# Kernel optimization log

Hardware: AMD Instinct MI355X
Metric: run time of the kernel (lower is better)

## Reference

```python
import jax, jax.numpy as jnp
import numpy as np

N_NODES = 100000
N_EDGES = 1600000
F_IN = 256
HID = 32
HEADS = 4
N_CLASS = 40
NEG_SLOPE = 0.2  # DGL GATConv default leaky_relu slope


def _gat_layer(x, src, dst, W, attn_l, attn_r, bias, num_nodes):
    """One DGL-style GATConv layer.
    x: [N, F_in]; W: [F_in, H*D]; attn_l/attn_r: [H, D]; bias: [H, D].
    Returns [N, H, D].
    """
    H, D = attn_l.shape
    h = (x @ W).reshape(-1, H, D)                      # [N, H, D]
    el = jnp.einsum('nhd,hd->nh', h, attn_l)           # [N, H]
    er = jnp.einsum('nhd,hd->nh', h, attn_r)           # [N, H]
    e = el[src] + er[dst]                              # [E, H]
    e = jnp.where(e > 0, e, NEG_SLOPE * e)             # leaky_relu
    # segment softmax over edges grouped by destination node
    m = jax.ops.segment_max(e, dst, num_segments=num_nodes)   # [N, H]
    ex = jnp.exp(e - m[dst])                           # [E, H]
    denom = jax.ops.segment_sum(ex, dst, num_segments=num_nodes)  # [N, H]
    alpha = ex / (denom[dst] + 1e-9)                   # [E, H]
    msg = h[src] * alpha[:, :, None]                   # [E, H, D]
    out = jax.ops.segment_sum(msg, dst, num_segments=num_nodes)   # [N, H, D]
    return out + bias[None, :, :]


def setup_inputs() -> dict:
    key = jax.random.key(0)
    ks = jax.random.split(key, 16)
    x = jax.random.normal(ks[0], (N_NODES, F_IN), dtype=jnp.float32)
    edge_src = jax.random.randint(ks[1], (N_EDGES,), 0, N_NODES, dtype=jnp.int32)
    edge_dst = jax.random.randint(ks[2], (N_EDGES,), 0, N_NODES, dtype=jnp.int32)

    def glorot(k, shape):
        fan_in, fan_out = shape[0], int(np.prod(shape[1:]))
        lim = float(np.sqrt(6.0 / (fan_in + fan_out)))
        return jax.random.uniform(k, shape, jnp.float32, -lim, lim)

    d1 = HID * HEADS  # 128
    inp = {
        'x': x, 'edge_src': edge_src, 'edge_dst': edge_dst,
        'W1': glorot(ks[3], (F_IN, HEADS * HID)),
        'al1': glorot(ks[4], (HEADS, HID)),
        'ar1': glorot(ks[5], (HEADS, HID)),
        'b1': jnp.zeros((HEADS, HID), jnp.float32),
        'W2': glorot(ks[6], (d1, HEADS * HID)),
        'al2': glorot(ks[7], (HEADS, HID)),
        'ar2': glorot(ks[8], (HEADS, HID)),
        'b2': jnp.zeros((HEADS, HID), jnp.float32),
        'W3': glorot(ks[9], (d1, 1 * N_CLASS)),
        'al3': glorot(ks[10], (1, N_CLASS)),
        'ar3': glorot(ks[11], (1, N_CLASS)),
        'b3': jnp.zeros((1, N_CLASS), jnp.float32),
    }
    return inp


def reference(x, edge_src, edge_dst, W1, al1, ar1, b1, W2, al2, ar2, b2, W3, al3, ar3, b3):
    N = x.shape[0]
    h = _gat_layer(x, edge_src, edge_dst, W1, al1, ar1, b1, N).reshape(N, -1)
    h = jax.nn.elu(h)  # act='elu'
    h = _gat_layer(h, edge_src, edge_dst, W2, al2, ar2, b2, N).reshape(N, -1)
    h = jax.nn.elu(h)
    out = _gat_layer(h, edge_src, edge_dst, W3, al3, ar3, b3, N).reshape(N, -1)
    return out
```

## Files before the change

### kernel.cpp

```cpp
#include <hip/hip_runtime.h>
#include <math.h>


#define HEADS 4
#define HID   32
#define NCLS  40
#define BSH   8
#define CH    4096
#define BCAP  6144

typedef __attribute__((ext_vector_type(8))) short bf16x8;
typedef __attribute__((ext_vector_type(4))) float f32x4;

static __device__ __forceinline__ unsigned short f2bf(float f) {
    unsigned int u = __float_as_uint(f);
    u += 0x7fffu + ((u >> 16) & 1u);
    return (unsigned short)(u >> 16);
}
static __device__ __forceinline__ float bflo(unsigned int v) {
    return __uint_as_float(v << 16);
}
static __device__ __forceinline__ float bfhi(unsigned int v) {
    return __uint_as_float(v & 0xffff0000u);
}
static __device__ __forceinline__ unsigned int pack2bf(float lo, float hi) {
    return (unsigned int)f2bf(lo) | ((unsigned int)f2bf(hi) << 16);
}


__global__ __launch_bounds__(256) void prep_all(const float* __restrict__ W1,
                                                const float* __restrict__ W2,
                                                const float* __restrict__ W3,
                                                unsigned short* __restrict__ Wt1,
                                                unsigned short* __restrict__ Wt2,
                                                unsigned short* __restrict__ Wt3,
                                                int NBUCK, int* __restrict__ bcur) {
    int g = blockIdx.x * 256 + threadIdx.x;
    if (g < 32768) {
        int m = g >> 8, k = g & 255;
        Wt1[g] = f2bf(W1[(size_t)k * 128 + m]);
    } else if (g < 49152) {
        int g2 = g - 32768;
        int m = g2 >> 7, k = g2 & 127;
        Wt2[g2] = f2bf(W2[(size_t)k * 128 + m]);
    } else if (g < 54272) {
        int g3 = g - 49152;
        int m = g3 >> 7, k = g3 & 127;
        Wt3[g3] = f2bf(W3[(size_t)k * 40 + m]);
    } else if (g - 54272 < NBUCK) {
        int b = g - 54272;
        bcur[b] = b * BCAP;
    }
}


__global__ __launch_bounds__(256) void bucket_partition(const int* __restrict__ src,
                                                        const int* __restrict__ dst, int E,
                                                        int NBUCK, int* __restrict__ bcur,
                                                        unsigned long long* __restrict__ ebuf) {
    __shared__ int h[512];
    __shared__ int base[512];
    int tid = threadIdx.x;
    int e0 = blockIdx.x * CH;
    for (int i = tid; i < NBUCK; i += 256) h[i] = 0;
    __syncthreads();
    #pragma unroll
    for (int l = 0; l < CH / 256; ++l) {
        int g = e0 + l * 256 + tid;
        if (g < E) atomicAdd(&h[dst[g] >> BSH], 1);
    }
    __syncthreads();
    for (int i = tid; i < NBUCK; i += 256) {
        int c = h[i];
        if (c) base[i] = atomicAdd(&bcur[i], c);
    }
    __syncthreads();
    #pragma unroll
    for (int l = 0; l < CH / 256; ++l) {
        int g = e0 + l * 256 + tid;
        if (g < E) {
            int d = dst[g];
            int p = atomicAdd(&base[d >> BSH], 1);
            ebuf[p] = ((unsigned long long)(unsigned)d << 32) | (unsigned)src[g];
        }
    }
}

__global__ __launch_bounds__(256) void bucket_csr(const unsigned long long* __restrict__ ebuf,
                                                  const int* __restrict__ bcur, int N,
                                                  int2* __restrict__ rowbe,
                                                  int* __restrict__ csrc) {
    __shared__ int cnt[256];
    __shared__ int s[256];
    int b = blockIdx.x, tid = threadIdx.x;
    int beg = b * BCAP, end = bcur[b];
    int d0 = b << BSH;
    cnt[tid] = 0;
    __syncthreads();
    for (int i = beg + tid; i < end; i += 256)
        atomicAdd(&cnt[(int)(ebuf[i] >> 32) - d0], 1);
    __syncthreads();
    int v = cnt[tid];
    s[tid] = v;
    __syncthreads();
    for (int off = 1; off < 256; off <<= 1) {
        int t = (tid >= off) ? s[tid - off] : 0;
        __syncthreads();
        s[tid] += t;
        __syncthreads();
    }
    int excl = s[tid] - v;
    int d = d0 + tid;
    if (d < N) rowbe[d] = make_int2(beg + excl, beg + excl + v);
    cnt[tid] = beg + excl;
    __syncthreads();
    for (int i = beg + tid; i < end; i += 256) {
        unsigned long long e = ebuf[i];
        int p = atomicAdd(&cnt[(int)(e >> 32) - d0], 1);
        csrc[p] = (int)(e & 0xffffffffu);
    }
}


template <bool AFP32, bool OBF, bool WIDEN>
__global__ __launch_bounds__(256) void gemm_mfma(const void* __restrict__ Asrc,
                                                 const unsigned short* __restrict__ Wt,
                                                 void* __restrict__ Y,
                                                 int N, int K, int M) {
    constexpr int WRF = WIDEN ? 4 : 2;
    constexpr int WCF = WIDEN ? 4 : 3;
    __shared__ __align__(16) unsigned short As[128][40];
    __shared__ __align__(16) unsigned short Bs[128][40];
    const int t = threadIdx.x;
    const int lane = t & 63, w = t >> 6;
    const int r0 = blockIdx.x * 128;
    const int wrow = WIDEN ? (w >> 1) * 64 : w * 32;
    const int wcol = WIDEN ? (w & 1) * 64 : 0;
    const int srow = t >> 1, shalf = t & 1;
    const int lr = lane & 15, lq = lane >> 4;
    f32x4 acc[WRF][WCF];
    #pragma unroll
    for (int f = 0; f < WRF; ++f)
        #pragma unroll
        for (int g = 0; g < WCF; ++g)
            acc[f][g] = (f32x4){0.f, 0.f, 0.f, 0.f};

    for (int k0 = 0; k0 < K; k0 += 32) {
        {
            int gr = r0 + srow;
            if (gr < N) {
                if constexpr (AFP32) {
                    const float* gp = (const float*)Asrc + (size_t)gr * K + k0 + shalf * 16;
                    float4 f0 = *(const float4*)(gp + 0);
                    float4 f1 = *(const float4*)(gp + 4);
                    float4 f2 = *(const float4*)(gp + 8);
                    float4 f3 = *(const float4*)(gp + 12);
                    *(uint4*)&As[srow][shalf * 16 + 0] =
                        make_uint4(pack2bf(f0.x, f0.y), pack2bf(f0.z, f0.w),
                                   pack2bf(f1.x, f1.y), pack2bf(f1.z, f1.w));
                    *(uint4*)&As[srow][shalf * 16 + 8] =
                        make_uint4(pack2bf(f2.x, f2.y), pack2bf(f2.z, f2.w),
                                   pack2bf(f3.x, f3.y), pack2bf(f3.z, f3.w));
                } else {
                    const uint4* gp = (const uint4*)((const unsigned short*)Asrc +
                                                     (size_t)gr * K + k0 + shalf * 16);
                    *(uint4*)&As[srow][shalf * 16 + 0] = gp[0];
                    *(uint4*)&As[srow][shalf * 16 + 8] = gp[1];
                }
            }
        }
        {
            int col = srow;
            if (col < M) {
                const uint4* gp = (const uint4*)(Wt + (size_t)col * K + k0 + shalf * 16);
                *(uint4*)&Bs[col][shalf * 16 + 0] = gp[0];
                *(uint4*)&Bs[col][shalf * 16 + 8] = gp[1];
            }
        }
        __syncthreads();
        bf16x8 af[WRF], bfr[WCF];
        #pragma unroll
        for (int f = 0; f < WRF; ++f)
            af[f] = *(const bf16x8*)&As[wrow + f * 16 + lr][lq * 8];
        #pragma unroll
        for (int g = 0; g < WCF; ++g)
            bfr[g] = *(const bf16x8*)&Bs[wcol + g * 16 + lr][lq * 8];
        #pragma unroll
        for (int f = 0; f < WRF; ++f)
            #pragma unroll
            for (int g = 0; g < WCF; ++g)
                acc[f][g] = __builtin_amdgcn_mfma_f32_16x16x32_bf16(af[f], bfr[g],
                                                                   acc[f][g], 0, 0, 0);
        __syncthreads();
    }
    #pragma unroll
    for (int f = 0; f < WRF; ++f) {
        #pragma unroll
        for (int g = 0; g < WCF; ++g) {
            int col = wcol + g * 16 + lr;
            if (!WIDEN && col >= M) continue;
            #pragma unroll
            for (int r = 0; r < 4; ++r) {
                int row = r0 + wrow + f * 16 + lq * 4 + r;
                if (row < N) {
                    if constexpr (OBF)
                        ((unsigned short*)Y)[(size_t)row * M + col] = f2bf(acc[f][g][r]);
                    else
                        ((float*)Y)[(size_t)row * M + col] = acc[f][g][r];
                }
            }
        }
    }
}


template <int H, int D, bool BF>
__global__ __launch_bounds__(256) void elr_kernel(const void* __restrict__ hv,
                                                  const float* __restrict__ al,
                                                  const float* __restrict__ ar,
                                                  float* __restrict__ el,
                                                  float* __restrict__ er, int N) {
    int g = blockIdx.x * blockDim.x + threadIdx.x;
    int n = g / H, hh = g % H;
    if (n >= N) return;
    float sl = 0.f, sr = 0.f;
    if constexpr (BF) {
        const unsigned short* hp = (const unsigned short*)hv + (size_t)n * H * D + hh * D;
        #pragma unroll
        for (int d = 0; d < D; d += 8) {
            uint4 u = *(const uint4*)(hp + d);
            float4 a0 = *(const float4*)(al + hh * D + d);
            float4 a1 = *(const float4*)(al + hh * D + d + 4);
            float4 r0 = *(const float4*)(ar + hh * D + d);
            float4 r1 = *(const float4*)(ar + hh * D + d + 4);
            float h0 = bflo(u.x), h1 = bfhi(u.x);
            float h2 = bflo(u.y), h3 = bfhi(u.y);
            float h4 = bflo(u.z), h5 = bfhi(u.z);
            float h6 = bflo(u.w), h7 = bfhi(u.w);
            sl += h0 * a0.x + h1 * a0.y + h2 * a0.z + h3 * a0.w
                + h4 * a1.x + h5 * a1.y + h6 * a1.z + h7 * a1.w;
            sr += h0 * r0.x + h1 * r0.y + h2 * r0.z + h3 * r0.w
                + h4 * r1.x + h5 * r1.y + h6 * r1.z + h7 * r1.w;
        }
    } else {
        const float* hp = (const float*)hv + (size_t)n * H * D + hh * D;
        #pragma unroll
        for (int d = 0; d < D; d += 4) {
            float4 hvv = *(const float4*)(hp + d);
            float4 av = *(const float4*)(al + hh * D + d);
            float4 rv = *(const float4*)(ar + hh * D + d);
            sl += hvv.x * av.x + hvv.y * av.y + hvv.z * av.z + hvv.w * av.w;
            sr += hvv.x * rv.x + hvv.y * rv.y + hvv.z * rv.z + hvv.w * rv.w;
        }
    }
    el[(size_t)n * H + hh] = sl;
    er[(size_t)n * H + hh] = sr;
}


template <int H, int D, bool ELU, bool BFW, bool OB>
__global__ __launch_bounds__(256) void agg_kernel(const void* __restrict__ hsrcv,
                                                  const float* __restrict__ el,
                                                  const float* __restrict__ er,
                                                  const float* __restrict__ bias,
                                                  const int2* __restrict__ rowbe,
                                                  const int* __restrict__ csrc,
                                                  void* __restrict__ outv, int N) {
    constexpr int HD = H * D;
    int wid = (int)(((size_t)blockIdx.x * blockDim.x + threadIdx.x) >> 6);
    int lane = threadIdx.x & 63;
    if (wid >= N) return;
    int eb = BFW ? lane * 2 : lane;
    bool active = BFW || (lane < HD);
    int head = active ? (eb / D) : 0;
    float er_d = er[(size_t)wid * H + head];
    int2 be = rowbe[wid];
    int beg = be.x, end = be.y;
    const unsigned int* hb = (const unsigned int*)hsrcv;
    const float* hf = (const float*)hsrcv;

    float denom = 0.f, a0 = 0.f, a1 = 0.f;

#define AGG_UPDATE(EV, HX, HY)                                                 \
    {                                                                          \
        float e_ = (EV) + er_d;                                                \
        e_ = (e_ > 0.f) ? e_ : 0.2f * e_;                                      \
        float ex_ = __expf(e_);                                                \
        denom += ex_;                                                          \
        a0 = fmaf(ex_, (HX), a0);                                              \
        a1 = fmaf(ex_, (HY), a1);                                              \
    }

    for (int chunk = beg; chunk < end; chunk += 64) {
        int cnt = min(64, end - chunk);
        int cs = (lane < cnt) ? csrc[chunk + lane] : 0;
        int j = 0;
        for (; j + 4 <= cnt; j += 4) {
            int s0 = __shfl(cs, j + 0), s1 = __shfl(cs, j + 1);
            int s2 = __shfl(cs, j + 2), s3 = __shfl(cs, j + 3);
            float e0 = el[(size_t)s0 * H + head];
            float e1 = el[(size_t)s1 * H + head];
            float e2 = el[(size_t)s2 * H + head];
            float e3 = el[(size_t)s3 * H + head];
            float h0x, h0y = 0.f, h1x, h1y = 0.f, h2x, h2y = 0.f, h3x, h3y = 0.f;
            if (BFW) {
                unsigned int v0 = hb[(size_t)s0 * (HD / 2) + lane];
                unsigned int v1 = hb[(size_t)s1 * (HD / 2) + lane];
                unsigned int v2 = hb[(size_t)s2 * (HD / 2) + lane];
                unsigned int v3 = hb[(size_t)s3 * (HD / 2) + lane];
                h0x = bflo(v0); h0y = bfhi(v0);
                h1x = bflo(v1); h1y = bfhi(v1);
                h2x = bflo(v2); h2y = bfhi(v2);
                h3x = bflo(v3); h3y = bfhi(v3);
            } else {
                h0x = active ? hf[(size_t)s0 * HD + eb] : 0.f;
                h1x = active ? hf[(size_t)s1 * HD + eb] : 0.f;
                h2x = active ? hf[(size_t)s2 * HD + eb] : 0.f;
                h3x = active ? hf[(size_t)s3 * HD + eb] : 0.f;
            }
            AGG_UPDATE(e0, h0x, h0y);
            AGG_UPDATE(e1, h1x, h1y);
            AGG_UPDATE(e2, h2x, h2y);
            AGG_UPDATE(e3, h3x, h3y);
        }
        for (; j < cnt; ++j) {
            int s0 = __shfl(cs, j);
            float e0 = el[(size_t)s0 * H + head];
            float hx, hy = 0.f;
            if (BFW) {
                unsigned int v0 = hb[(size_t)s0 * (HD / 2) + lane];
                hx = bflo(v0); hy = bfhi(v0);
            } else {
                hx = active ? hf[(size_t)s0 * HD + eb] : 0.f;
            }
            AGG_UPDATE(e0, hx, hy);
        }
    }
#undef AGG_UPDATE

    float inv = 1.f / (denom + 1e-9f);
    if (BFW) {
        float o0 = a0 * inv + bias[eb];
        float o1 = a1 * inv + bias[eb + 1];
        if (ELU) {
            o0 = (o0 > 0.f) ? o0 : expm1f(o0);
            o1 = (o1 > 0.f) ? o1 : expm1f(o1);
        }
        if constexpr (OB) {
            ((unsigned int*)outv)[(size_t)wid * (HD / 2) + lane] = pack2bf(o0, o1);
        } else {
            *(float2*)((float*)outv + (size_t)wid * HD + eb) = make_float2(o0, o1);
        }
    } else if (active) {
        float o = a0 * inv + bias[eb];
        if (ELU) o = (o > 0.f) ? o : expm1f(o);
        ((float*)outv)[(size_t)wid * HD + eb] = o;
    }
}


extern "C" void kernel_launch(void* const* d_in, const int* in_sizes, int n_in,
                              void* d_out, int out_size, void* d_ws, size_t ws_size,
                              hipStream_t stream) {
    const float* x    = (const float*)d_in[0];
    const int* esrc   = (const int*)d_in[1];
    const int* edst   = (const int*)d_in[2];
    const float* W1   = (const float*)d_in[3];
    const float* al1  = (const float*)d_in[4];
    const float* ar1  = (const float*)d_in[5];
    const float* b1   = (const float*)d_in[6];
    const float* W2   = (const float*)d_in[7];
    const float* al2  = (const float*)d_in[8];
    const float* ar2  = (const float*)d_in[9];
    const float* b2   = (const float*)d_in[10];
    const float* W3   = (const float*)d_in[11];
    const float* al3  = (const float*)d_in[12];
    const float* ar3  = (const float*)d_in[13];
    const float* b3   = (const float*)d_in[14];

    const int FIN = 256;
    const int N = in_sizes[0] / FIN;
    const int E = in_sizes[1];
    const int D1 = HEADS * HID;
    const int NBUCK = (N + 255) >> BSH;

    unsigned short* Abf = (unsigned short*)d_ws;
    unsigned short* Cbf = Abf + (size_t)N * D1;
    float* A32 = (float*)(Cbf + (size_t)N * D1);
    float* el  = A32 + (size_t)N * NCLS;
    float* er  = el + (size_t)N * HEADS;
    int2* rowbe = (int2*)(er + (size_t)N * HEADS);
    int* csrc   = (int*)(rowbe + N);
    int* bcur   = csrc + (size_t)NBUCK * BCAP;
    unsigned short* Wt1 = (unsigned short*)(bcur + NBUCK);
    unsigned short* Wt2 = Wt1 + 128 * 256;
    unsigned short* Wt3 = Wt2 + 128 * 128;
    unsigned long long* ebuf = (unsigned long long*)Abf;

    int WGRID = (int)(((size_t)N * 64 + 255) / 256);
    int PB = (E + CH - 1) / CH;
    int GB = (N + 127) / 128;

    prep_all<<<(54272 + NBUCK + 255) / 256, 256, 0, stream>>>(W1, W2, W3, Wt1, Wt2, Wt3,
                                                              NBUCK, bcur);

    bucket_partition<<<PB, 256, 0, stream>>>(esrc, edst, E, NBUCK, bcur, ebuf);
    bucket_csr<<<NBUCK, 256, 0, stream>>>(ebuf, bcur, N, rowbe, csrc);

    gemm_mfma<true, true, true><<<GB, 256, 0, stream>>>(x, Wt1, Abf, N, FIN, D1);
    elr_kernel<HEADS, HID, true><<<(N * HEADS + 255) / 256, 256, 0, stream>>>(Abf, al1, ar1, el, er, N);
    agg_kernel<HEADS, HID, true, true, true><<<WGRID, 256, 0, stream>>>(Abf, el, er, b1, rowbe, csrc, Cbf, N);

    gemm_mfma<false, true, true><<<GB, 256, 0, stream>>>(Cbf, Wt2, Abf, N, D1, D1);
    elr_kernel<HEADS, HID, true><<<(N * HEADS + 255) / 256, 256, 0, stream>>>(Abf, al2, ar2, el, er, N);
    agg_kernel<HEADS, HID, true, true, true><<<WGRID, 256, 0, stream>>>(Abf, el, er, b2, rowbe, csrc, Cbf, N);

    gemm_mfma<false, false, false><<<GB, 256, 0, stream>>>(Cbf, Wt3, A32, N, D1, NCLS);
    elr_kernel<1, NCLS, false><<<(N + 255) / 256, 256, 0, stream>>>(A32, al3, ar3, el, er, N);
    agg_kernel<1, NCLS, false, false, false><<<WGRID, 256, 0, stream>>>(A32, el, er, b3, rowbe, csrc, d_out, N);
}
```

Baseline: 363.1 us.

## Fold attention projections into GEMM weights and double-buffer GEMM LDS tiles

```diff
diff --git a/kernel.cpp b/kernel.cpp
--- a/kernel.cpp
+++ b/kernel.cpp
@@ -31,24 +31,56 @@
 __global__ __launch_bounds__(256) void prep_all(const float* __restrict__ W1,
                                                 const float* __restrict__ W2,
                                                 const float* __restrict__ W3,
+                                                const float* __restrict__ al1,
+                                                const float* __restrict__ ar1,
+                                                const float* __restrict__ al2,
+                                                const float* __restrict__ ar2,
+                                                const float* __restrict__ al3,
+                                                const float* __restrict__ ar3,
                                                 unsigned short* __restrict__ Wt1,
                                                 unsigned short* __restrict__ Wt2,
                                                 unsigned short* __restrict__ Wt3,
+                                                unsigned short* __restrict__ aw1,
+                                                unsigned short* __restrict__ aw2,
+                                                unsigned short* __restrict__ aw3,
                                                 int NBUCK, int* __restrict__ bcur) {
     int g = blockIdx.x * 256 + threadIdx.x;
     if (g < 32768) {
         int m = g >> 8, k = g & 255;
         Wt1[g] = f2bf(W1[(size_t)k * 128 + m]);
     } else if (g < 49152) {
-        int g2 = g - 32768;
-        int m = g2 >> 7, k = g2 & 127;
-        Wt2[g2] = f2bf(W2[(size_t)k * 128 + m]);
+        int i = g - 32768;
+        int m = i >> 7, k = i & 127;
+        Wt2[i] = f2bf(W2[(size_t)k * 128 + m]);
     } else if (g < 54272) {
-        int g3 = g - 49152;
-        int m = g3 >> 7, k = g3 & 127;
-        Wt3[g3] = f2bf(W3[(size_t)k * 40 + m]);
-    } else if (g - 54272 < NBUCK) {
-        int b = g - 54272;
+        int i = g - 49152;
+        int m = i >> 7, k = i & 127;
+        Wt3[i] = f2bf(W3[(size_t)k * 40 + m]);
+    } else if (g < 56320) {
+        int i = g - 54272;
+        int v = i >> 8, k = i & 255;
+        const float* a = (v < 4) ? al1 : ar1;
+        int h = v & 3;
+        float s = 0.f;
+        for (int d = 0; d < 32; ++d) s += W1[(size_t)k * 128 + h * 32 + d] * a[h * 32 + d];
+        aw1[v * 256 + k] = f2bf(s);
+    } else if (g < 57344) {
+        int i = g - 56320;
+        int v = i >> 7, k = i & 127;
+        const float* a = (v < 4) ? al2 : ar2;
+        int h = v & 3;
+        float s = 0.f;
+        for (int d = 0; d < 32; ++d) s += W2[(size_t)k * 128 + h * 32 + d] * a[h * 32 + d];
+        aw2[v * 128 + k] = f2bf(s);
+    } else if (g < 57600) {
+        int i = g - 57344;
+        int v = i >> 7, k = i & 127;
+        const float* a = v ? ar3 : al3;
+        float s = 0.f;
+        for (int m = 0; m < 40; ++m) s += W3[(size_t)k * 40 + m] * a[m];
+        aw3[v * 128 + k] = f2bf(s);
+    } else if (g - 57600 < NBUCK) {
+        int b = g - 57600;
         bcur[b] = b * BCAP;
     }
 }
@@ -125,12 +157,17 @@
 template <bool AFP32, bool OBF, bool WIDEN>
 __global__ __launch_bounds__(256) void gemm_mfma(const void* __restrict__ Asrc,
                                                  const unsigned short* __restrict__ Wt,
+                                                 const unsigned short* __restrict__ aw,
                                                  void* __restrict__ Y,
+                                                 float* __restrict__ el,
+                                                 float* __restrict__ er,
                                                  int N, int K, int M) {
     constexpr int WRF = WIDEN ? 4 : 2;
     constexpr int WCF = WIDEN ? 4 : 3;
-    __shared__ __align__(16) unsigned short As[128][40];
-    __shared__ __align__(16) unsigned short Bs[128][40];
+    constexpr int BR  = WIDEN ? 144 : 48;
+    constexpr int EBASE = WIDEN ? 128 : 0;
+    __shared__ __align__(16) unsigned short As[2][128][40];
+    __shared__ __align__(16) unsigned short Bs[2][BR][40];
     const int t = threadIdx.x;
     const int lane = t & 63, w = t >> 6;
     const int r0 = blockIdx.x * 128;
@@ -138,123 +175,144 @@
     const int wcol = WIDEN ? (w & 1) * 64 : 0;
     const int srow = t >> 1, shalf = t & 1;
     const int lr = lane & 15, lq = lane >> 4;
+    const bool xw = WIDEN && (w & 1);
+    const int gr = r0 + srow;
+    const bool arow_ok = gr < N;
+    const bool brow_ok = srow < (WIDEN ? M : M + 2);
+
     f32x4 acc[WRF][WCF];
     #pragma unroll
     for (int f = 0; f < WRF; ++f)
         #pragma unroll
         for (int g = 0; g < WCF; ++g)
             acc[f][g] = (f32x4){0.f, 0.f, 0.f, 0.f};
-
-    for (int k0 = 0; k0 < K; k0 += 32) {
-        {
-            int gr = r0 + srow;
-            if (gr < N) {
-                if constexpr (AFP32) {
-                    const float* gp = (const float*)Asrc + (size_t)gr * K + k0 + shalf * 16;
-                    float4 f0 = *(const float4*)(gp + 0);
-                    float4 f1 = *(const float4*)(gp + 4);
-                    float4 f2 = *(const float4*)(gp + 8);
-                    float4 f3 = *(const float4*)(gp + 12);
-                    *(uint4*)&As[srow][shalf * 16 + 0] =
-                        make_uint4(pack2bf(f0.x, f0.y), pack2bf(f0.z, f0.w),
-                                   pack2bf(f1.x, f1.y), pack2bf(f1.z, f1.w));
-                    *(uint4*)&As[srow][shalf * 16 + 8] =
-                        make_uint4(pack2bf(f2.x, f2.y), pack2bf(f2.z, f2.w),
-                                   pack2bf(f3.x, f3.y), pack2bf(f3.z, f3.w));
-                } else {
-                    const uint4* gp = (const uint4*)((const unsigned short*)Asrc +
-                                                     (size_t)gr * K + k0 + shalf * 16);
-                    *(uint4*)&As[srow][shalf * 16 + 0] = gp[0];
-                    *(uint4*)&As[srow][shalf * 16 + 8] = gp[1];
-                }
-            }
-        }
-        {
-            int col = srow;
-            if (col < M) {
-                const uint4* gp = (const uint4*)(Wt + (size_t)col * K + k0 + shalf * 16);
-                *(uint4*)&Bs[col][shalf * 16 + 0] = gp[0];
-                *(uint4*)&Bs[col][shalf * 16 + 8] = gp[1];
-            }
-        }
-        __syncthreads();
-        bf16x8 af[WRF], bfr[WCF];
+    f32x4 acc4[WRF];
+    #pragma unroll
+    for (int f = 0; f < WRF; ++f) acc4[f] = (f32x4){0.f, 0.f, 0.f, 0.f};
+
+    const int nsteps = K >> 5;
+    float4 xf0 = {0,0,0,0}, xf1 = {0,0,0,0}, xf2 = {0,0,0,0}, xf3 = {0,0,0,0};
+    uint4 xu0 = {0,0,0,0}, xu1 = {0,0,0,0};
+    uint4 bu0, bu1, eu0, eu1;
+
+#define G_LOAD(K0)                                                                       \
+    {                                                                                    \
+        if (arow_ok) {                                                                   \
+            if constexpr (AFP32) {                                                       \
+                const float* gp = (const float*)Asrc + (size_t)gr * K + (K0) + shalf*16; \
+                xf0 = *(const float4*)(gp + 0);  xf1 = *(const float4*)(gp + 4);         \
+                xf2 = *(const float4*)(gp + 8);  xf3 = *(const float4*)(gp + 12);        \
+            } else {                                                                     \
+                const uint4* gp = (const uint4*)((const unsigned short*)Asrc +           \
+                                                 (size_t)gr * K + (K0) + shalf * 16);    \
+                xu0 = gp[0]; xu1 = gp[1];                                                \
+            }                                                                            \
+        }                                                                                \
+        if (brow_ok) {                                                                   \
+            const unsigned short* bp = (srow < M) ? (Wt + (size_t)srow * K)              \
+                                                  : (aw + (size_t)(srow - M) * K);       \
+            const uint4* gp = (const uint4*)(bp + (K0) + shalf * 16);                    \
+            bu0 = gp[0]; bu1 = gp[1];                                                    \
+        }                                                                                \
+        if (WIDEN && t < 16) {                                                           \
+            const uint4* gp = (const uint4*)(aw + (size_t)(t >> 1) * K + (K0) + (t & 1) * 16); \
+            eu0 = gp[0]; eu1 = gp[1];                                                    \
+        }                                                                                \
+    }
+
+#define L_STORE(B)                                                                       \
+    {                                                                                    \
+        if constexpr (AFP32) {                                                           \
+            *(uint4*)&As[B][srow][shalf * 16 + 0] =                                      \
+                make_uint4(pack2bf(xf0.x, xf0.y), pack2bf(xf0.z, xf0.w),                 \
+                           pack2bf(xf1.x, xf1.y), pack2bf(xf1.z, xf1.w));                \
+            *(uint4*)&As[B][srow][shalf * 16 + 8] =                                      \
+                make_uint4(pack2bf(xf2.x, xf2.y), pack2bf(xf2.z, xf2.w),                 \
+                           pack2bf(xf3.x, xf3.y), pack2bf(xf3.z, xf3.w));                \
+        } else {                                                                         \
+            *(uint4*)&As[B][srow][shalf * 16 + 0] = xu0;                                 \
+            *(uint4*)&As[B][srow][shalf * 16 + 8] = xu1;                                 \
+        }                                                                                \
+        if (brow_ok) {                                                                   \
+            *(uint4*)&Bs[B][srow][shalf * 16 + 0] = bu0;                                 \
+            *(uint4*)&Bs[B][srow][shalf * 16 + 8] = bu1;                                 \
+        }                                                                                \
+        if (WIDEN && t < 16) {                                                           \
+            *(uint4*)&Bs[B][EBASE + (t >> 1)][(t & 1) * 16 + 0] = eu0;                   \
+            *(uint4*)&Bs[B][EBASE + (t >> 1)][(t & 1) * 16 + 8] = eu1;                   \
+        }                                                                                \
+    }
+
+    G_LOAD(0);
+    L_STORE(0);
+    __syncthreads();
+    for (int s = 0; s < nsteps; ++s) {
+        const int cur = s & 1;
+        if (s + 1 < nsteps) G_LOAD((s + 1) * 32);
+        bf16x8 af[WRF], bfr[WCF], ef;
         #pragma unroll
         for (int f = 0; f < WRF; ++f)
-            af[f] = *(const bf16x8*)&As[wrow + f * 16 + lr][lq * 8];
+            af[f] = *(const bf16x8*)&As[cur][wrow + f * 16 + lr][lq * 8];
         #pragma unroll
         for (int g = 0; g < WCF; ++g)
-            bfr[g] = *(const bf16x8*)&Bs[wcol + g * 16 + lr][lq * 8];
+            bfr[g] = *(const bf16x8*)&Bs[cur][wcol + g * 16 + lr][lq * 8];
+        if (xw) ef = *(const bf16x8*)&Bs[cur][EBASE + lr][lq * 8];
         #pragma unroll
         for (int f = 0; f < WRF; ++f)
             #pragma unroll
             for (int g = 0; g < WCF; ++g)
                 acc[f][g] = __builtin_amdgcn_mfma_f32_16x16x32_bf16(af[f], bfr[g],
-                                                                   acc[f][g], 0, 0, 0);
+                                                                    acc[f][g], 0, 0, 0);
+        if (xw) {
+            #pragma unroll
+            for (int f = 0; f < WRF; ++f)
+                acc4[f] = __builtin_amdgcn_mfma_f32_16x16x32_bf16(af[f], ef,
+                                                                  acc4[f], 0, 0, 0);
+        }
+        if (s + 1 < nsteps) L_STORE(cur ^ 1);
         __syncthreads();
     }
+#undef G_LOAD
+#undef L_STORE
+
     #pragma unroll
     for (int f = 0; f < WRF; ++f) {
         #pragma unroll
         for (int g = 0; g < WCF; ++g) {
             int col = wcol + g * 16 + lr;
-            if (!WIDEN && col >= M) continue;
             #pragma unroll
             for (int r = 0; r < 4; ++r) {
                 int row = r0 + wrow + f * 16 + lq * 4 + r;
-                if (row < N) {
+                if (row >= N) continue;
+                if (WIDEN || col < M) {
                     if constexpr (OBF)
                         ((unsigned short*)Y)[(size_t)row * M + col] = f2bf(acc[f][g][r]);
                     else
                         ((float*)Y)[(size_t)row * M + col] = acc[f][g][r];
+                } else if (col == M) {
+                    el[row] = acc[f][g][r];
+                } else if (col == M + 1) {
+                    er[row] = acc[f][g][r];
                 }
             }
         }
     }
-}
-
-
-template <int H, int D, bool BF>
-__global__ __launch_bounds__(256) void elr_kernel(const void* __restrict__ hv,
-                                                  const float* __restrict__ al,
-                                                  const float* __restrict__ ar,
-                                                  float* __restrict__ el,
-                                                  float* __restrict__ er, int N) {
-    int g = blockIdx.x * blockDim.x + threadIdx.x;
-    int n = g / H, hh = g % H;
-    if (n >= N) return;
-    float sl = 0.f, sr = 0.f;
-    if constexpr (BF) {
-        const unsigned short* hp = (const unsigned short*)hv + (size_t)n * H * D + hh * D;
-        #pragma unroll
-        for (int d = 0; d < D; d += 8) {
-            uint4 u = *(const uint4*)(hp + d);
-            float4 a0 = *(const float4*)(al + hh * D + d);
-            float4 a1 = *(const float4*)(al + hh * D + d + 4);
-            float4 r0 = *(const float4*)(ar + hh * D + d);
-            float4 r1 = *(const float4*)(ar + hh * D + d + 4);
-            float h0 = bflo(u.x), h1 = bfhi(u.x);
-            float h2 = bflo(u.y), h3 = bfhi(u.y);
-            float h4 = bflo(u.z), h5 = bfhi(u.z);
-            float h6 = bflo(u.w), h7 = bfhi(u.w);
-            sl += h0 * a0.x + h1 * a0.y + h2 * a0.z + h3 * a0.w
-                + h4 * a1.x + h5 * a1.y + h6 * a1.z + h7 * a1.w;
-            sr += h0 * r0.x + h1 * r0.y + h2 * r0.z + h3 * r0.w
-                + h4 * r1.x + h5 * r1.y + h6 * r1.z + h7 * r1.w;
-        }
-    } else {
-        const float* hp = (const float*)hv + (size_t)n * H * D + hh * D;
-        #pragma unroll
-        for (int d = 0; d < D; d += 4) {
-            float4 hvv = *(const float4*)(hp + d);
-            float4 av = *(const float4*)(al + hh * D + d);
-            float4 rv = *(const float4*)(ar + hh * D + d);
-            sl += hvv.x * av.x + hvv.y * av.y + hvv.z * av.z + hvv.w * av.w;
-            sr += hvv.x * rv.x + hvv.y * rv.y + hvv.z * rv.z + hvv.w * rv.w;
-        }
-    }
-    el[(size_t)n * H + hh] = sl;
-    er[(size_t)n * H + hh] = sr;
+    if constexpr (WIDEN) {
+        if (xw && lr < 8) {
+            #pragma unroll
+            for (int f = 0; f < WRF; ++f) {
+                #pragma unroll
+                for (int r = 0; r < 4; ++r) {
+                    int row = r0 + wrow + f * 16 + lq * 4 + r;
+                    if (row < N) {
+                        float v = acc4[f][r];
+                        if (lr < 4) el[(size_t)row * 4 + lr] = v;
+                        else        er[(size_t)row * 4 + (lr - 4)] = v;
+                    }
+                }
+            }
+        }
+    }
 }
 
 
@@ -383,6 +441,7 @@
     const int E = in_sizes[1];
     const int D1 = HEADS * HID;
     const int NBUCK = (N + 255) >> BSH;
+    const int NBUCKP = 392;
 
     unsigned short* Abf = (unsigned short*)d_ws;
     unsigned short* Cbf = Abf + (size_t)N * D1;
@@ -392,30 +451,31 @@
     int2* rowbe = (int2*)(er + (size_t)N * HEADS);
     int* csrc   = (int*)(rowbe + N);
     int* bcur   = csrc + (size_t)NBUCK * BCAP;
-    unsigned short* Wt1 = (unsigned short*)(bcur + NBUCK);
+    unsigned short* Wt1 = (unsigned short*)(bcur + NBUCKP);
     unsigned short* Wt2 = Wt1 + 128 * 256;
     unsigned short* Wt3 = Wt2 + 128 * 128;
+    unsigned short* aw1 = Wt3 + 40 * 128;
+    unsigned short* aw2 = aw1 + 8 * 256;
+    unsigned short* aw3 = aw2 + 8 * 128;
     unsigned long long* ebuf = (unsigned long long*)Abf;
 
     int WGRID = (int)(((size_t)N * 64 + 255) / 256);
     int PB = (E + CH - 1) / CH;
     int GB = (N + 127) / 128;
 
-    prep_all<<<(54272 + NBUCK + 255) / 256, 256, 0, stream>>>(W1, W2, W3, Wt1, Wt2, Wt3,
-                                                              NBUCK, bcur);
+    prep_all<<<(57600 + NBUCK + 255) / 256, 256, 0, stream>>>(
+        W1, W2, W3, al1, ar1, al2, ar2, al3, ar3,
+        Wt1, Wt2, Wt3, aw1, aw2, aw3, NBUCK, bcur);
 
     bucket_partition<<<PB, 256, 0, stream>>>(esrc, edst, E, NBUCK, bcur, ebuf);
     bucket_csr<<<NBUCK, 256, 0, stream>>>(ebuf, bcur, N, rowbe, csrc);
 
-    gemm_mfma<true, true, true><<<GB, 256, 0, stream>>>(x, Wt1, Abf, N, FIN, D1);
-    elr_kernel<HEADS, HID, true><<<(N * HEADS + 255) / 256, 256, 0, stream>>>(Abf, al1, ar1, el, er, N);
+    gemm_mfma<true, true, true><<<GB, 256, 0, stream>>>(x, Wt1, aw1, Abf, el, er, N, FIN, D1);
     agg_kernel<HEADS, HID, true, true, true><<<WGRID, 256, 0, stream>>>(Abf, el, er, b1, rowbe, csrc, Cbf, N);
 
-    gemm_mfma<false, true, true><<<GB, 256, 0, stream>>>(Cbf, Wt2, Abf, N, D1, D1);
-    elr_kernel<HEADS, HID, true><<<(N * HEADS + 255) / 256, 256, 0, stream>>>(Abf, al2, ar2, el, er, N);
+    gemm_mfma<false, true, true><<<GB, 256, 0, stream>>>(Cbf, Wt2, aw2, Abf, el, er, N, D1, D1);
     agg_kernel<HEADS, HID, true, true, true><<<WGRID, 256, 0, stream>>>(Abf, el, er, b2, rowbe, csrc, Cbf, N);
 
-    gemm_mfma<false, false, false><<<GB, 256, 0, stream>>>(Cbf, Wt3, A32, N, D1, NCLS);
-    elr_kernel<1, NCLS, false><<<(N + 255) / 256, 256, 0, stream>>>(A32, al3, ar3, el, er, N);
+    gemm_mfma<false, false, false><<<GB, 256, 0, stream>>>(Cbf, Wt3, aw3, A32, el, er, N, D1, NCLS);
     agg_kernel<1, NCLS, false, false, false><<<WGRID, 256, 0, stream>>>(A32, el, er, b3, rowbe, csrc, d_out, N);
 }
```

Result: faster. 327.3 us (-9.9%).
